# Kernel tuning notes

Measured on AMD Instinct MI355X. Metric: run time of the kernel, lower is better.

The kernel has to match this reference:

```python
import jax, jax.numpy as jnp
import numpy as np

B, IN, OUT, F, COMP = 8192, 4096, 4096, 16, 1024
FS = IN // F  # fragment_size = 256


def setup_inputs() -> dict:
    key = jax.random.key(0)
    k1, k2, k3, k4, k5 = jax.random.split(key, 5)
    x = jax.random.normal(k1, (B, IN), dtype=jnp.float32)
    selector_weights = jax.random.normal(k2, (F, FS), dtype=jnp.float32) / np.sqrt(FS)
    expert_weights = jax.random.normal(k3, (F, FS, OUT), dtype=jnp.float32) / np.sqrt(FS)
    # nn.Linear default init ~ U(-1/sqrt(fan_in), 1/sqrt(fan_in)); scale is irrelevant for correctness
    W_comp = jax.random.normal(k4, (COMP, IN), dtype=jnp.float32) / np.sqrt(IN)
    W_net = jax.random.normal(k5, (OUT, COMP), dtype=jnp.float32) / np.sqrt(COMP)
    return {"x": x, "selector_weights": selector_weights, "expert_weights": expert_weights,
            "W_comp": W_comp, "W_net": W_net}


def reference(x, selector_weights, expert_weights, W_comp, W_net):
    # Training-mode forward: soft top-fragment gating + dense compress path.
    b, in_f = x.shape
    f, fs = selector_weights.shape
    xf = x.reshape(b, f, fs)                                  # [B, F, FS]
    scores = jnp.einsum('bfi,fi->bf', xf, selector_weights)   # [B, F]
    probs = jax.nn.softmax(scores, axis=1)                    # [B, F]
    # gated grouped matmul: sum_f probs[b,f] * (x_f @ W_f)
    expert_out = jnp.einsum('bfi,fio,bf->bo', xf, expert_weights, probs)  # [B, OUT]
    # mask = 1 - probs expanded per-feature (fragment_mapping = repeat_interleave)
    mask = 1.0 - jnp.repeat(probs, fs, axis=1)                # [B, IN]
    masked = x * mask
    compressed = masked @ W_comp.T                            # [B, COMP]
    out = compressed @ W_net.T + expert_out                   # [B, OUT]
    return out
```

## Files before the change

kernel.cpp:

```cpp
#include <hip/hip_runtime.h>
#include <hip/hip_bf16.h>
#include <cstdint>
#include <cstddef>

#define B_    8192
#define IN_   4096
#define OUT_  4096
#define F_    16
#define FS_   256
#define COMP_ 1024
#define KBIG  (IN_ + COMP_)

typedef unsigned short ushort_t;
typedef __attribute__((ext_vector_type(8))) short short8;
typedef __attribute__((ext_vector_type(4))) float f32x4;

__device__ __forceinline__ ushort_t f2b(float f) {
  unsigned u = __float_as_uint(f);
  u += 0x7fffu + ((u >> 16) & 1u);
  return (ushort_t)(u >> 16);
}

__device__ __forceinline__ void gll16(const void* gp, void* lp) {
  __builtin_amdgcn_global_load_lds(
      (const __attribute__((address_space(1))) unsigned int*)gp,
      (__attribute__((address_space(3))) unsigned int*)lp, 16, 0, 0);
}

__global__ void __launch_bounds__(256) gate_kernel(
    const float* __restrict__ x, const float* __restrict__ sel,
    ushort_t* __restrict__ Abig, ushort_t* __restrict__ Mbuf) {
  const int row = blockIdx.x;
  const int t = threadIdx.x;
  const float* xr = x + (size_t)row * IN_ + t * 16;
  float4 xv0 = ((const float4*)xr)[0];
  float4 xv1 = ((const float4*)xr)[1];
  float4 xv2 = ((const float4*)xr)[2];
  float4 xv3 = ((const float4*)xr)[3];

  const int f = t >> 4;
  const int sub = t & 15;
  const float* sp = sel + f * FS_ + sub * 16;
  float4 s0 = ((const float4*)sp)[0];
  float4 s1 = ((const float4*)sp)[1];
  float4 s2 = ((const float4*)sp)[2];
  float4 s3 = ((const float4*)sp)[3];

  float dot = xv0.x * s0.x + xv0.y * s0.y + xv0.z * s0.z + xv0.w * s0.w
            + xv1.x * s1.x + xv1.y * s1.y + xv1.z * s1.z + xv1.w * s1.w
            + xv2.x * s2.x + xv2.y * s2.y + xv2.z * s2.z + xv2.w * s2.w
            + xv3.x * s3.x + xv3.y * s3.y + xv3.z * s3.z + xv3.w * s3.w;

  #pragma unroll
  for (int off = 8; off; off >>= 1) dot += __shfl_xor(dot, off, 64);

  __shared__ float sc[F_];
  if (sub == 0) sc[f] = dot;
  __syncthreads();

  float mx = sc[0];
  #pragma unroll
  for (int i = 1; i < F_; ++i) mx = fmaxf(mx, sc[i]);
  float sum = 0.f;
  #pragma unroll
  for (int i = 0; i < F_; ++i) sum += __expf(sc[i] - mx);
  const float p = __expf(sc[f] - mx) / sum;

  float xs[16] = {xv0.x, xv0.y, xv0.z, xv0.w, xv1.x, xv1.y, xv1.z, xv1.w,
                  xv2.x, xv2.y, xv2.z, xv2.w, xv3.x, xv3.y, xv3.z, xv3.w};
  union { ushort_t u[8]; uint4 v; } a0, a1, m0, m1;
  #pragma unroll
  for (int j = 0; j < 8; ++j) {
    float y0 = xs[j] * p;
    float y1 = xs[8 + j] * p;
    a0.u[j] = f2b(y0);
    a1.u[j] = f2b(y1);
    m0.u[j] = f2b(xs[j] - y0);
    m1.u[j] = f2b(xs[8 + j] - y1);
  }
  ushort_t* ap = Abig + (size_t)row * KBIG + t * 16;
  *(uint4*)ap = a0.v;
  *(uint4*)(ap + 8) = a1.v;
  ushort_t* mp = Mbuf + (size_t)row * IN_ + t * 16;
  *(uint4*)mp = m0.v;
  *(uint4*)(mp + 8) = m1.v;
}

__global__ void __launch_bounds__(256) conv_expertT(
    const float* __restrict__ We, ushort_t* __restrict__ Bbig) {
  __shared__ float tile[64][65];
  const int k0 = blockIdx.x * 64;
  const int o0 = blockIdx.y * 64;
  const int t = threadIdx.x;
  const int kr = t >> 4;
  const int oq = t & 15;
  #pragma unroll
  for (int rr = 0; rr < 4; ++rr) {
    int k = rr * 16 + kr;
    float4 v = *(const float4*)(We + (size_t)(k0 + k) * OUT_ + o0 + oq * 4);
    tile[k][oq * 4 + 0] = v.x;
    tile[k][oq * 4 + 1] = v.y;
    tile[k][oq * 4 + 2] = v.z;
    tile[k][oq * 4 + 3] = v.w;
  }
  __syncthreads();
  const int kc = t & 7;
  #pragma unroll
  for (int rr = 0; rr < 2; ++rr) {
    int o = rr * 32 + (t >> 3);
    union { ushort_t u[8]; uint4 v; } w;
    #pragma unroll
    for (int j = 0; j < 8; ++j) w.u[j] = f2b(tile[kc * 8 + j][o]);
    *(uint4*)(Bbig + (size_t)(o0 + o) * KBIG + k0 + kc * 8) = w.v;
  }
}

__global__ void __launch_bounds__(256) conv_net(
    const float* __restrict__ Wnet, ushort_t* __restrict__ Bbig) {
  int tid = blockIdx.x * 256 + threadIdx.x;
  int base = tid * 8;
  int o = base >> 10;
  int c = base & (COMP_ - 1);
  float4 v0 = ((const float4*)(Wnet + base))[0];
  float4 v1 = ((const float4*)(Wnet + base))[1];
  union { ushort_t u[8]; uint4 v; } w;
  w.u[0] = f2b(v0.x); w.u[1] = f2b(v0.y); w.u[2] = f2b(v0.z); w.u[3] = f2b(v0.w);
  w.u[4] = f2b(v1.x); w.u[5] = f2b(v1.y); w.u[6] = f2b(v1.z); w.u[7] = f2b(v1.w);
  *(uint4*)(Bbig + (size_t)o * KBIG + IN_ + c) = w.v;
}

__global__ void __launch_bounds__(256) conv_comp(
    const float* __restrict__ Wc, ushort_t* __restrict__ Wcb) {
  int tid = blockIdx.x * 256 + threadIdx.x;
  int base = tid * 8;
  float4 v0 = ((const float4*)(Wc + base))[0];
  float4 v1 = ((const float4*)(Wc + base))[1];
  union { ushort_t u[8]; uint4 v; } w;
  w.u[0] = f2b(v0.x); w.u[1] = f2b(v0.y); w.u[2] = f2b(v0.z); w.u[3] = f2b(v0.w);
  w.u[4] = f2b(v1.x); w.u[5] = f2b(v1.y); w.u[6] = f2b(v1.z); w.u[7] = f2b(v1.w);
  *(uint4*)(Wcb + base) = w.v;
}

__global__ void __launch_bounds__(256) reduce_split(
    const float* __restrict__ p0, const float* __restrict__ p1,
    ushort_t* __restrict__ Abig) {
  int tid = blockIdx.x * 256 + threadIdx.x;
  float4 a = ((const float4*)p0)[tid];
  float4 b = ((const float4*)p1)[tid];
  int row = tid >> 8;
  int c4 = tid & 255;
  union { ushort_t u[4]; uint2 v; } w;
  w.u[0] = f2b(a.x + b.x);
  w.u[1] = f2b(a.y + b.y);
  w.u[2] = f2b(a.z + b.z);
  w.u[3] = f2b(a.w + b.w);
  *(uint2*)(Abig + (size_t)row * KBIG + IN_ + c4 * 4) = w.v;
}

template <bool BF16_OUT>
__global__ void __launch_bounds__(512, 2) gemm256(
    const ushort_t* __restrict__ A, int lda,
    const ushort_t* __restrict__ Bt, int ldb,
    int KS, void* __restrict__ Cp, int ldc, int num_pid_n,
    int num_pid, size_t coff) {
  __shared__ __align__(16) ushort_t As[2 * 256 * 64];
  __shared__ __align__(16) ushort_t Bs[2 * 256 * 64];
  const int t = threadIdx.x;
  const int wave = t >> 6;
  const int lane = t & 63;

  const int s = blockIdx.x / num_pid;
  int rem_all = blockIdx.x - s * num_pid;
  A += (size_t)s * KS;
  Bt += (size_t)s * KS;

  rem_all = (rem_all & 7) * (num_pid >> 3) + (rem_all >> 3);

  const int pids_per_group = num_pid_n << 4;
  const int group_id = rem_all / pids_per_group;
  const int rem = rem_all - group_id * pids_per_group;
  const int pid_m = (group_id << 4) + (rem & 15);
  const int pid_n = rem >> 4;

  const int wr = (wave >> 2) * 128;
  const int wc = (wave & 3) * 64;

  const int lr = lane >> 3;
  const int gch = (lane & 7) ^ lr;
  const ushort_t* gA = A + (size_t)(pid_m * 256 + wave * 8 + lr) * lda + gch * 8;
  const ushort_t* gB = Bt + (size_t)(pid_n * 256 + wave * 8 + lr) * ldb + gch * 8;
  const size_t a64 = (size_t)64 * lda;
  const size_t b64 = (size_t)64 * ldb;
  ushort_t* lA = As + wave * 512;
  ushort_t* lB = Bs + wave * 512;

  #define STAGE_A(BF, H, KT) do {                                          \
    const ushort_t* g_ = gA + (size_t)(KT) * 64 + (size_t)(2 * (H)) * a64; \
    ushort_t* d_ = lA + (BF) * 16384 + (H) * 8192;                         \
    gll16(g_, d_);                                                         \
    gll16(g_ + a64, d_ + 4096); } while (0)
  #define STAGE_B(BF, H, KT) do {                                          \
    const ushort_t* g_ = gB + (size_t)(KT) * 64 + (size_t)(2 * (H)) * b64; \
    ushort_t* d_ = lB + (BF) * 16384 + (H) * 8192;                         \
    gll16(g_, d_);                                                         \
    gll16(g_ + b64, d_ + 4096); } while (0)

  const int r = lane & 15;
  const int q = lane >> 4;
  const int sw = r & 7;
  const int sl0 = (q ^ sw) * 8;
  const int sl1 = ((q + 4) ^ sw) * 8;
  const ushort_t* aRd = As + (wr >> 7) * 8192 + r * 64;
  const ushort_t* bRd = Bs + (wc >> 7) * 8192 + (wc & 64) * 64 + r * 64;

  const int nt = KS >> 6;

  f32x4 acc[8][4] = {};
  short8 a[4][2], b[4][2];

  #define MFMA_PH(MB, NB) do {                                            \
    __builtin_amdgcn_s_setprio(1);                                        \
    _Pragma("unroll")                                                     \
    for (int mi = 0; mi < 4; ++mi) {                                      \
      _Pragma("unroll")                                                   \
      for (int nj = 0; nj < 2; ++nj) {                                    \
        _Pragma("unroll")                                                 \
        for (int ks = 0; ks < 2; ++ks)                                    \
          acc[(MB) + mi][(NB) + nj] =                                     \
              __builtin_amdgcn_mfma_f32_16x16x32_bf16(                    \
                  a[mi][ks], b[(NB) + nj][ks], acc[(MB) + mi][(NB) + nj], \
                  0, 0, 0);                                               \
      }                                                                   \
    }                                                                     \
    __builtin_amdgcn_s_setprio(0); } while (0)

  #define WAIT_LGKM0() do {                                               \
    asm volatile("s_waitcnt lgkmcnt(0)" ::: "memory");                    \
    __builtin_amdgcn_sched_barrier(0); } while (0)

  STAGE_A(0, 0, 0); STAGE_A(0, 1, 0);
  STAGE_B(0, 0, 0); STAGE_B(0, 1, 0);
  if (nt > 1) {
    STAGE_B(1, 0, 1); STAGE_B(1, 1, 1);
    asm volatile("s_waitcnt vmcnt(4)" ::: "memory");
  } else {
    asm volatile("s_waitcnt vmcnt(0)" ::: "memory");
  }
  __builtin_amdgcn_sched_barrier(0);
  __builtin_amdgcn_s_barrier();

  for (int kt = 0; kt < nt; ++kt) {
    const int bf = kt & 1;
    const int nb = bf ^ 1;
    const ushort_t* aB = aRd + bf * 16384;
    const ushort_t* bB = bRd + bf * 16384;
    const bool p1ok = kt + 1 < nt;
    const bool p2ok = kt + 2 < nt;

    #pragma unroll
    for (int mi = 0; mi < 4; ++mi) {
      a[mi][0] = *(const short8*)(aB + mi * 1024 + sl0);
      a[mi][1] = *(const short8*)(aB + mi * 1024 + sl1);
    }
    #pragma unroll
    for (int nj = 0; nj < 2; ++nj) {
      b[nj][0] = *(const short8*)(bB + nj * 1024 + sl0);
      b[nj][1] = *(const short8*)(bB + nj * 1024 + sl1);
    }
    if (p1ok) STAGE_A(nb, 0, kt + 1);
    __builtin_amdgcn_s_barrier();
    WAIT_LGKM0();
    MFMA_PH(0, 0);
    __builtin_amdgcn_s_barrier();

    #pragma unroll
    for (int nj = 2; nj < 4; ++nj) {
      b[nj][0] = *(const short8*)(bB + nj * 1024 + sl0);
      b[nj][1] = *(const short8*)(bB + nj * 1024 + sl1);
    }
    if (p1ok) STAGE_A(nb, 1, kt + 1);
    __builtin_amdgcn_s_barrier();
    WAIT_LGKM0();
    MFMA_PH(0, 2);
    __builtin_amdgcn_s_barrier();

    #pragma unroll
    for (int mi = 0; mi < 4; ++mi) {
      a[mi][0] = *(const short8*)(aB + (mi + 4) * 1024 + sl0);
      a[mi][1] = *(const short8*)(aB + (mi + 4) * 1024 + sl1);
    }
    if (p2ok) STAGE_B(bf, 0, kt + 2);
    __builtin_amdgcn_s_barrier();
    WAIT_LGKM0();
    MFMA_PH(4, 0);
    __builtin_amdgcn_s_barrier();

    if (p2ok) STAGE_B(bf, 1, kt + 2);
    __builtin_amdgcn_s_barrier();
    MFMA_PH(4, 2);
    if (p2ok) asm volatile("s_waitcnt vmcnt(4)" ::: "memory");
    else      asm volatile("s_waitcnt vmcnt(0)" ::: "memory");
    __builtin_amdgcn_sched_barrier(0);
    __builtin_amdgcn_s_barrier();
  }

  const int row0 = pid_m * 256 + wr + q * 4;
  const int col0 = pid_n * 256 + wc + r;
  #pragma unroll
  for (int mi = 0; mi < 8; ++mi) {
    #pragma unroll
    for (int ni = 0; ni < 4; ++ni) {
      const int row = row0 + mi * 16;
      const int col = col0 + ni * 16;
      #pragma unroll
      for (int rr = 0; rr < 4; ++rr) {
        float v = acc[mi][ni][rr];
        if (BF16_OUT)
          ((ushort_t*)Cp)[(size_t)(row + rr) * ldc + col + s * coff] = f2b(v);
        else
          ((float*)Cp)[(size_t)(row + rr) * ldc + col + s * coff] = v;
      }
    }
  }
  #undef STAGE_A
  #undef STAGE_B
  #undef MFMA_PH
  #undef WAIT_LGKM0
}

extern "C" void kernel_launch(void* const* d_in, const int* in_sizes, int n_in,
                              void* d_out, int out_size, void* d_ws, size_t ws_size,
                              hipStream_t stream) {
  const float* x     = (const float*)d_in[0];
  const float* sel   = (const float*)d_in[1];
  const float* We    = (const float*)d_in[2];
  const float* Wcomp = (const float*)d_in[3];
  const float* Wnet  = (const float*)d_in[4];
  float* out = (float*)d_out;

  char* ws = (char*)d_ws;
  const size_t szAbig = (size_t)B_ * KBIG * 2;
  const size_t szMbuf = (size_t)B_ * IN_ * 2;
  const size_t szBbig = (size_t)OUT_ * KBIG * 2;
  ushort_t* Abig = (ushort_t*)ws;
  ushort_t* Mbuf = (ushort_t*)(ws + szAbig);
  ushort_t* Bbig = (ushort_t*)(ws + szAbig + szMbuf);
  ushort_t* Wcb  = (ushort_t*)(ws + szAbig + szMbuf + szBbig);

  float* part0 = out;
  float* part1 = out + (size_t)B_ * COMP_;

  gate_kernel<<<B_, 256, 0, stream>>>(x, sel, Abig, Mbuf);

  conv_expertT<<<dim3(IN_ / 64, OUT_ / 64), 256, 0, stream>>>(We, Bbig);
  conv_net<<<(OUT_ * COMP_) / (256 * 8), 256, 0, stream>>>(Wnet, Bbig);
  conv_comp<<<(COMP_ * IN_) / (256 * 8), 256, 0, stream>>>(Wcomp, Wcb);

  gemm256<false><<<2 * (B_ / 256) * (COMP_ / 256), 512, 0, stream>>>(
      Mbuf, IN_, Wcb, IN_, IN_ / 2, (void*)part0, COMP_, COMP_ / 256,
      (B_ / 256) * (COMP_ / 256), (size_t)B_ * COMP_);
  reduce_split<<<(B_ * COMP_) / (256 * 4), 256, 0, stream>>>(part0, part1, Abig);

  gemm256<false><<<(B_ / 256) * (OUT_ / 256), 512, 0, stream>>>(
      Abig, KBIG, Bbig, KBIG, KBIG, (void*)out, OUT_, OUT_ / 256,
      (B_ / 256) * (OUT_ / 256), 0);
}
```

Measured before the change: 725.4 us.

## Software-pipeline LDS fragment reads across k-iterations in GEMM main loop

The first A/B register fragments for the next k-tile are now read from LDS at the end of the previous iteration, and the waits are relaxed to partial lgkmcnt/vmcnt counts. The goal is to overlap LDS reads with MFMA work and to take the initial LDS latency off the critical path of each iteration. This reorders the waits and barriers inside a double-buffered schedule, which risks races on the LDS buffers if the counts are wrong. It also adds register pressure.

```diff
diff --git a/kernel.cpp b/kernel.cpp
--- a/kernel.cpp
+++ b/kernel.cpp
@@ -234,10 +234,6 @@
     }                                                                     \
     __builtin_amdgcn_s_setprio(0); } while (0)
 
-  #define WAIT_LGKM0() do {                                               \
-    asm volatile("s_waitcnt lgkmcnt(0)" ::: "memory");                    \
-    __builtin_amdgcn_sched_barrier(0); } while (0)
-
   STAGE_A(0, 0, 0); STAGE_A(0, 1, 0);
   STAGE_B(0, 0, 0); STAGE_B(0, 1, 0);
   if (nt > 1) {
@@ -248,59 +244,82 @@
   }
   __builtin_amdgcn_sched_barrier(0);
   __builtin_amdgcn_s_barrier();
+  #pragma unroll
+  for (int mi = 0; mi < 4; ++mi) {
+    a[mi][0] = *(const short8*)(aRd + mi * 1024 + sl0);
+    a[mi][1] = *(const short8*)(aRd + mi * 1024 + sl1);
+  }
+  #pragma unroll
+  for (int nj = 0; nj < 2; ++nj) {
+    b[nj][0] = *(const short8*)(bRd + nj * 1024 + sl0);
+    b[nj][1] = *(const short8*)(bRd + nj * 1024 + sl1);
+  }
 
   for (int kt = 0; kt < nt; ++kt) {
     const int bf = kt & 1;
     const int nb = bf ^ 1;
-    const ushort_t* aB = aRd + bf * 16384;
-    const ushort_t* bB = bRd + bf * 16384;
+    const ushort_t* aB  = aRd + bf * 16384;
+    const ushort_t* bB  = bRd + bf * 16384;
+    const ushort_t* aBn = aRd + nb * 16384;
+    const ushort_t* bBn = bRd + nb * 16384;
     const bool p1ok = kt + 1 < nt;
     const bool p2ok = kt + 2 < nt;
-
-    #pragma unroll
-    for (int mi = 0; mi < 4; ++mi) {
-      a[mi][0] = *(const short8*)(aB + mi * 1024 + sl0);
-      a[mi][1] = *(const short8*)(aB + mi * 1024 + sl1);
-    }
-    #pragma unroll
-    for (int nj = 0; nj < 2; ++nj) {
-      b[nj][0] = *(const short8*)(bB + nj * 1024 + sl0);
-      b[nj][1] = *(const short8*)(bB + nj * 1024 + sl1);
-    }
-    if (p1ok) STAGE_A(nb, 0, kt + 1);
-    __builtin_amdgcn_s_barrier();
-    WAIT_LGKM0();
-    MFMA_PH(0, 0);
-    __builtin_amdgcn_s_barrier();
 
     #pragma unroll
     for (int nj = 2; nj < 4; ++nj) {
       b[nj][0] = *(const short8*)(bB + nj * 1024 + sl0);
       b[nj][1] = *(const short8*)(bB + nj * 1024 + sl1);
     }
+    if (p1ok) STAGE_A(nb, 0, kt + 1);
+    __builtin_amdgcn_s_barrier();
+    asm volatile("s_waitcnt lgkmcnt(4)" ::: "memory");
+    __builtin_amdgcn_sched_barrier(0);
+    MFMA_PH(0, 0);
+    __builtin_amdgcn_s_barrier();
+
     if (p1ok) STAGE_A(nb, 1, kt + 1);
     __builtin_amdgcn_s_barrier();
-    WAIT_LGKM0();
+    asm volatile("s_waitcnt lgkmcnt(0)" ::: "memory");
+    __builtin_amdgcn_sched_barrier(0);
     MFMA_PH(0, 2);
-    __builtin_amdgcn_s_barrier();
-
     #pragma unroll
     for (int mi = 0; mi < 4; ++mi) {
       a[mi][0] = *(const short8*)(aB + (mi + 4) * 1024 + sl0);
       a[mi][1] = *(const short8*)(aB + (mi + 4) * 1024 + sl1);
     }
-    if (p2ok) STAGE_B(bf, 0, kt + 2);
-    __builtin_amdgcn_s_barrier();
-    WAIT_LGKM0();
+    __builtin_amdgcn_sched_barrier(0);
+    __builtin_amdgcn_s_barrier();
+
+    if (p2ok) {
+      STAGE_B(bf, 0, kt + 2);
+      asm volatile("s_waitcnt vmcnt(2)" ::: "memory");
+    } else {
+      asm volatile("s_waitcnt vmcnt(0)" ::: "memory");
+    }
+    __builtin_amdgcn_sched_barrier(0);
+    __builtin_amdgcn_s_barrier();
+    asm volatile("s_waitcnt lgkmcnt(0)" ::: "memory");
+    __builtin_amdgcn_sched_barrier(0);
     MFMA_PH(4, 0);
     __builtin_amdgcn_s_barrier();
 
     if (p2ok) STAGE_B(bf, 1, kt + 2);
     __builtin_amdgcn_s_barrier();
+    __builtin_amdgcn_sched_barrier(0);
     MFMA_PH(4, 2);
-    if (p2ok) asm volatile("s_waitcnt vmcnt(4)" ::: "memory");
-    else      asm volatile("s_waitcnt vmcnt(0)" ::: "memory");
-    __builtin_amdgcn_sched_barrier(0);
+    if (p1ok) {
+      #pragma unroll
+      for (int mi = 0; mi < 4; ++mi) {
+        a[mi][0] = *(const short8*)(aBn + mi * 1024 + sl0);
+        a[mi][1] = *(const short8*)(aBn + mi * 1024 + sl1);
+      }
+      #pragma unroll
+      for (int nj = 0; nj < 2; ++nj) {
+        b[nj][0] = *(const short8*)(bBn + nj * 1024 + sl0);
+        b[nj][1] = *(const short8*)(bBn + nj * 1024 + sl1);
+      }
+      __builtin_amdgcn_sched_barrier(0);
+    }
     __builtin_amdgcn_s_barrier();
   }
 
@@ -325,7 +344,6 @@
   #undef STAGE_A
   #undef STAGE_B
   #undef MFMA_PH
-  #undef WAIT_LGKM0
 }
 
 extern "C" void kernel_launch(void* const* d_in, const int* in_sizes, int n_in,
```

After: 841.3 us. 1.16x slower.
